# Kernel tuning notes

Hardware: AMD Instinct MI355X
Metric: run time of the kernel (lower is better)

The kernel has to match this reference:

```python
import jax, jax.numpy as jnp
import numpy as np

H, D = 4, 64          # num_heads, hidden_dim
NL, NP, B = 40000, 40000, 64
E_LL, E_LP, E_PL = 160000, 240000, 240000
NEG_SLOPE = 0.2


def _gat(x_src, x_dst, src, dst, Ws, Wd, al, ar, bias, n_dst):
    """DGL GATConv: fc -> edge score -> segment softmax over dst -> scatter-add."""
    fs = (x_src @ Ws).reshape(-1, H, D)            # [Ns,H,D]
    fd = (x_dst @ Wd).reshape(-1, H, D)            # [Nd,H,D]
    el = jnp.sum(fs * al, axis=-1)                 # [Ns,H]
    er = jnp.sum(fd * ar, axis=-1)                 # [Nd,H]
    e = jax.nn.leaky_relu(el[src] + er[dst], NEG_SLOPE)   # [E,H]
    m = jax.lax.stop_gradient(jax.ops.segment_max(e, dst, num_segments=n_dst))
    ex = jnp.exp(e - m[dst])
    s = jax.ops.segment_sum(ex, dst, num_segments=n_dst)
    a = ex / s[dst]                                # edge softmax over in-neighborhoods
    out = jax.ops.segment_sum(fs[src] * a[:, :, None], dst, num_segments=n_dst)
    return out + bias.reshape(1, H, D)


def _gmean(h, gid, nseg):
    s = jax.ops.segment_sum(h, gid, num_segments=nseg)
    c = jax.ops.segment_sum(jnp.ones((h.shape[0], 1), h.dtype), gid, num_segments=nseg)
    return s / jnp.maximum(c, 1.0)


_PARAM_SHAPES = [('W1_ll', (74, 256)), ('al1_ll', (H, D)), ('ar1_ll', (H, D)), ('b1_ll', (256,)),
                 ('W1_lps', (74, 256)), ('W1_lpd', (128, 256)), ('al1_lp', (H, D)), ('ar1_lp', (H, D)), ('b1_lp', (256,)),
                 ('W1_pls', (128, 256)), ('W1_pld', (74, 256)), ('al1_pl', (H, D)), ('ar1_pl', (H, D)), ('b1_pl', (256,)),
                 ('W2_ll', (256, 256)), ('al2_ll', (H, D)), ('ar2_ll', (H, D)), ('b2_ll', (256,)),
                 ('W2_lps', (256, 256)), ('W2_lpd', (256, 256)), ('al2_lp', (H, D)), ('ar2_lp', (H, D)), ('b2_lp', (256,)),
                 ('W2_pls', (256, 256)), ('W2_pld', (256, 256)), ('al2_pl', (H, D)), ('ar2_pl', (H, D)), ('b2_pl', (256,)),
                 ('W_mlp', (512, 256)), ('b_mlp', (256,))]


def setup_inputs() -> dict:
    key = jax.random.key(0)
    ks = iter(jax.random.split(key, 64))
    inp = {}
    inp['x_lig'] = jax.random.normal(next(ks), (NL, 74), jnp.float32)
    inp['x_pro'] = jax.random.normal(next(ks), (NP, 128), jnp.float32)
    for name, shape in _PARAM_SHAPES:
        inp[name] = jax.random.normal(next(ks), shape, jnp.float32) * 0.1
    inp['src_ll'] = jax.random.randint(next(ks), (E_LL,), 0, NL)
    inp['dst_ll'] = jax.random.randint(next(ks), (E_LL,), 0, NL)
    inp['src_lp'] = jax.random.randint(next(ks), (E_LP,), 0, NL)
    inp['dst_lp'] = jax.random.randint(next(ks), (E_LP,), 0, NP)
    inp['src_pl'] = jax.random.randint(next(ks), (E_PL,), 0, NP)
    inp['dst_pl'] = jax.random.randint(next(ks), (E_PL,), 0, NL)
    inp['gid_lig'] = jax.random.randint(next(ks), (NL,), 0, B)
    inp['gid_pro'] = jax.random.randint(next(ks), (NP,), 0, B)
    return inp


def reference(x_lig, x_pro, W1_ll, al1_ll, ar1_ll, b1_ll, W1_lps, W1_lpd, al1_lp, ar1_lp, b1_lp,
              W1_pls, W1_pld, al1_pl, ar1_pl, b1_pl, W2_ll, al2_ll, ar2_ll, b2_ll,
              W2_lps, W2_lpd, al2_lp, ar2_lp, b2_lp, W2_pls, W2_pld, al2_pl, ar2_pl, b2_pl,
              W_mlp, b_mlp, src_ll, dst_ll, src_lp, dst_lp, src_pl, dst_pl, gid_lig, gid_pro):
    # HeteroGraphConv layer 1 (aggregate='sum' over relations per dst ntype)
    h_l = (_gat(x_lig, x_lig, src_ll, dst_ll, W1_ll, W1_ll, al1_ll, ar1_ll, b1_ll, NL)
           + _gat(x_pro, x_lig, src_pl, dst_pl, W1_pls, W1_pld, al1_pl, ar1_pl, b1_pl, NL))
    h_p = _gat(x_lig, x_pro, src_lp, dst_lp, W1_lps, W1_lpd, al1_lp, ar1_lp, b1_lp, NP)
    h_l = jax.nn.relu(h_l.reshape(NL, H * D))
    h_p = jax.nn.relu(h_p.reshape(NP, H * D))
    # HeteroGraphConv layer 2
    h_l2 = (_gat(h_l, h_l, src_ll, dst_ll, W2_ll, W2_ll, al2_ll, ar2_ll, b2_ll, NL)
            + _gat(h_p, h_l, src_pl, dst_pl, W2_pls, W2_pld, al2_pl, ar2_pl, b2_pl, NL))
    h_p2 = _gat(h_l, h_p, src_lp, dst_lp, W2_lps, W2_lpd, al2_lp, ar2_lp, b2_lp, NP)
    h_l2 = jax.nn.relu(h_l2.reshape(NL, H * D))
    h_p2 = jax.nn.relu(h_p2.reshape(NP, H * D))
    # per-graph mean readout (dgl.mean_nodes) + concat + MLP (dropout=eval identity)
    g = jnp.concatenate([_gmean(h_l2, gid_lig, B), _gmean(h_p2, gid_pro, B)], axis=1)  # [B,512]
    return jax.nn.relu(g @ W_mlp + b_mlp)
```

## Files before the change

### kernel.cpp

```cpp
#include <hip/hip_runtime.h>
#include <hip/hip_bf16.h>

#define NLIG 40000
#define NPRO 40000
#define NGRAPH 64
#define ELL 160000
#define ELP 240000
#define EPL 240000

#define RD_STRIPES 256

typedef __hip_bfloat16 bf16;
typedef __attribute__((ext_vector_type(8))) short short8;
typedef __attribute__((ext_vector_type(4))) short short4v;
typedef __attribute__((ext_vector_type(4))) float f32x4;

__device__ __forceinline__ float bits2f(short s) {
  const unsigned u = ((unsigned)(unsigned short)s) << 16;
  return __uint_as_float(u);
}

__global__ __launch_bounds__(256) void convA_kernel(
    const float* __restrict__ A, bf16* __restrict__ hi, bf16* __restrict__ lo,
    int M, int K, int Kp) {
  const int row = blockIdx.x * 8 + (threadIdx.x >> 5);
  if (row >= M) return;
  const int Kp4 = Kp >> 2;
  short* hp = (short*)hi;
  short* lq = (short*)lo;
  for (int c4 = threadIdx.x & 31; c4 < Kp4; c4 += 32) {
    const int k = c4 << 2;
    float v[4];
#pragma unroll
    for (int j = 0; j < 4; ++j) {
      const int kk = k + j;
      v[j] = (kk < K) ? A[(size_t)row * K + kk] : 0.f;
    }
    short4v hv, lv;
#pragma unroll
    for (int j = 0; j < 4; ++j) {
      bf16 h = __float2bfloat16(v[j]);
      float r = v[j] - __bfloat162float(h);
      bf16 l = __float2bfloat16(r);
      hv[j] = *reinterpret_cast<short*>(&h);
      lv[j] = *reinterpret_cast<short*>(&l);
    }
    *reinterpret_cast<short4v*>(&hp[(size_t)row * Kp + k]) = hv;
    *reinterpret_cast<short4v*>(&lq[(size_t)row * Kp + k]) = lv;
  }
}

__global__ __launch_bounds__(256) void convBt_kernel(
    const float* __restrict__ B, bf16* __restrict__ thi, bf16* __restrict__ tlo,
    int K, int Kp) {
  const int tot = 256 * Kp;
  for (int i = blockIdx.x * 256 + threadIdx.x; i < tot; i += gridDim.x * 256) {
    const int n = i / Kp, k = i % Kp;
    float v = (k < K) ? B[(size_t)k * 256 + n] : 0.f;
    bf16 h = __float2bfloat16(v);
    float r = v - __bfloat162float(h);
    thi[i] = h;
    tlo[i] = __float2bfloat16(r);
  }
}

#define LP 40
__global__ __launch_bounds__(256) void mfma_gemm(
    const bf16* __restrict__ AhiP, const bf16* __restrict__ AloP,
    const bf16* __restrict__ BthiP, const bf16* __restrict__ BtloP,
    bf16* __restrict__ C, int M, int Kp,
    const float* __restrict__ al, float* __restrict__ el,
    const float* __restrict__ ar, float* __restrict__ er) {
  __shared__ short sA[2][128 * LP];
  __shared__ short sB[2][128 * LP];
  const short* Ahi = (const short*)AhiP;
  const short* Alo = (const short*)AloP;
  const short* Bthi = (const short*)BthiP;
  const short* Btlo = (const short*)BtloP;
  const int bid = blockIdx.x;
  const int rt = (bid >> 4) * 8 + (bid & 7);
  const int m0 = rt * 128;
  if (m0 >= M) return;
  const int n0 = ((bid >> 3) & 1) * 128;
  const int t = threadIdx.x;
  const int w = t >> 6, l = t & 63;
  const f32x4 zf = {0.f, 0.f, 0.f, 0.f};
  const short8 zs = {0, 0, 0, 0, 0, 0, 0, 0};
  f32x4 acc[2][8];
#pragma unroll
  for (int i = 0; i < 2; ++i)
#pragma unroll
    for (int j = 0; j < 8; ++j) acc[i][j] = zf;

  const int fr = l & 15, kg = l >> 4;

  for (int k0 = 0; k0 < Kp; k0 += 32) {
#pragma unroll
    for (int rep = 0; rep < 2; ++rep) {
      const int p = t + rep * 256;
      const int row = p >> 2, c = p & 3;
      const int gr = m0 + row;
      short8 vh = zs, vl = zs;
      if (gr < M) {
        const size_t g = (size_t)gr * Kp + k0 + c * 8;
        vh = *(const short8*)(Ahi + g);
        vl = *(const short8*)(Alo + g);
      }
      *(short8*)(&sA[0][row * LP + c * 8]) = vh;
      *(short8*)(&sA[1][row * LP + c * 8]) = vl;
    }
#pragma unroll
    for (int rep = 0; rep < 2; ++rep) {
      const int p = t + rep * 256;
      const int row = p >> 2, c = p & 3;
      const size_t g = (size_t)(n0 + row) * Kp + k0 + c * 8;
      *(short8*)(&sB[0][row * LP + c * 8]) = *(const short8*)(Bthi + g);
      *(short8*)(&sB[1][row * LP + c * 8]) = *(const short8*)(Btlo + g);
    }
    __syncthreads();
    short8 aF[2][2];
#pragma unroll
    for (int i = 0; i < 2; ++i) {
      const int r = (w * 32 + i * 16 + fr) * LP + kg * 8;
      aF[0][i] = *(const short8*)(&sA[0][r]);
      aF[1][i] = *(const short8*)(&sA[1][r]);
    }
#pragma unroll
    for (int j = 0; j < 8; ++j) {
      const int r = (j * 16 + fr) * LP + kg * 8;
      const short8 b0 = *(const short8*)(&sB[0][r]);
      const short8 b1 = *(const short8*)(&sB[1][r]);
#pragma unroll
      for (int i = 0; i < 2; ++i) {
        acc[i][j] = __builtin_amdgcn_mfma_f32_16x16x32_bf16(aF[0][i], b0, acc[i][j], 0, 0, 0);
        acc[i][j] = __builtin_amdgcn_mfma_f32_16x16x32_bf16(aF[0][i], b1, acc[i][j], 0, 0, 0);
        acc[i][j] = __builtin_amdgcn_mfma_f32_16x16x32_bf16(aF[1][i], b0, acc[i][j], 0, 0, 0);
      }
    }
    __syncthreads();
  }

#pragma unroll
  for (int i = 0; i < 2; ++i) {
    const int rbase = m0 + w * 32 + i * 16 + kg * 4;
#pragma unroll
    for (int j = 0; j < 8; ++j) {
      const int col = n0 + j * 16 + fr;
#pragma unroll
      for (int r = 0; r < 4; ++r) {
        const int row = rbase + r;
        if (row < M) C[(size_t)row * 256 + col] = __float2bfloat16(acc[i][j][r]);
      }
    }
  }

  if (el) {
    float alv[8], arv[8];
#pragma unroll
    for (int j = 0; j < 8; ++j) {
      alv[j] = al[n0 + j * 16 + fr];
      arv[j] = er ? ar[n0 + j * 16 + fr] : 0.f;
    }
    const int hb = n0 >> 6;
#pragma unroll
    for (int i = 0; i < 2; ++i) {
#pragma unroll
      for (int r = 0; r < 4; ++r) {
        float sl0 = 0.f, sl1 = 0.f, sr0 = 0.f, sr1 = 0.f;
#pragma unroll
        for (int j = 0; j < 4; ++j) {
          sl0 = fmaf(acc[i][j][r], alv[j], sl0);
          sr0 = fmaf(acc[i][j][r], arv[j], sr0);
          sl1 = fmaf(acc[i][j + 4][r], alv[j + 4], sl1);
          sr1 = fmaf(acc[i][j + 4][r], arv[j + 4], sr1);
        }
        sl0 += __shfl_xor(sl0, 1); sl0 += __shfl_xor(sl0, 2);
        sl0 += __shfl_xor(sl0, 4); sl0 += __shfl_xor(sl0, 8);
        sl1 += __shfl_xor(sl1, 1); sl1 += __shfl_xor(sl1, 2);
        sl1 += __shfl_xor(sl1, 4); sl1 += __shfl_xor(sl1, 8);
        sr0 += __shfl_xor(sr0, 1); sr0 += __shfl_xor(sr0, 2);
        sr0 += __shfl_xor(sr0, 4); sr0 += __shfl_xor(sr0, 8);
        sr1 += __shfl_xor(sr1, 1); sr1 += __shfl_xor(sr1, 2);
        sr1 += __shfl_xor(sr1, 4); sr1 += __shfl_xor(sr1, 8);
        const int row = m0 + w * 32 + i * 16 + kg * 4 + r;
        if (fr == 0 && row < M) {
          el[row * 4 + hb] = sl0;
          el[row * 4 + hb + 1] = sl1;
          if (er) {
            er[row * 4 + hb] = sr0;
            er[row * 4 + hb + 1] = sr1;
          }
        }
      }
    }
  }
}

__global__ void make_wr_kernel(const float* __restrict__ Wd,
                               const float* __restrict__ ar,
                               float* __restrict__ wr, int K) {
  const int t = blockIdx.x * blockDim.x + threadIdx.x;
  if (t < K * 4) {
    const int k = t >> 2, h = t & 3;
    float s = 0.f;
    for (int d = 0; d < 64; ++d)
      s = fmaf(Wd[(size_t)k * 256 + h * 64 + d], ar[h * 64 + d], s);
    wr[t] = s;
  }
}

__global__ __launch_bounds__(256) void er_gemv_kernel(
    const float* __restrict__ X, const float* __restrict__ wr,
    float* __restrict__ er, int n, int K) {
  __shared__ float swr[1024];
  const int t = threadIdx.x;
  for (int i = t; i < K * 4; i += blockDim.x) swr[i] = wr[i];
  __syncthreads();
  const int lane = t & 63;
  const int gw = (blockIdx.x * blockDim.x + t) >> 6;
  if (gw >= n) return;
  float a0 = 0.f, a1 = 0.f, a2 = 0.f, a3 = 0.f;
  for (int k = lane; k < K; k += 64) {
    const float x = X[(size_t)gw * K + k];
    a0 = fmaf(x, swr[k * 4 + 0], a0);
    a1 = fmaf(x, swr[k * 4 + 1], a1);
    a2 = fmaf(x, swr[k * 4 + 2], a2);
    a3 = fmaf(x, swr[k * 4 + 3], a3);
  }
#pragma unroll
  for (int o = 32; o; o >>= 1) {
    a0 += __shfl_xor(a0, o);
    a1 += __shfl_xor(a1, o);
    a2 += __shfl_xor(a2, o);
    a3 += __shfl_xor(a3, o);
  }
  if (lane == 0) {
    er[gw * 4 + 0] = a0; er[gw * 4 + 1] = a1;
    er[gw * 4 + 2] = a2; er[gw * 4 + 3] = a3;
  }
}

__global__ void count_kernel(const int* __restrict__ dst, int* __restrict__ cnt, int E) {
  for (int i = blockIdx.x * blockDim.x + threadIdx.x; i < E; i += gridDim.x * blockDim.x)
    atomicAdd(&cnt[dst[i]], 1);
}

__global__ __launch_bounds__(256) void scan_reduce_kernel(
    const int* __restrict__ data, int* __restrict__ bsum, int n) {
  const int base = blockIdx.x * 1024;
  int s = 0;
  for (int i = threadIdx.x; i < 1024; i += 256) {
    const int idx = base + i;
    s += (idx < n) ? data[idx] : 0;
  }
#pragma unroll
  for (int o = 32; o; o >>= 1) s += __shfl_xor(s, o);
  __shared__ int ws[4];
  if ((threadIdx.x & 63) == 0) ws[threadIdx.x >> 6] = s;
  __syncthreads();
  if (threadIdx.x == 0) bsum[blockIdx.x] = ws[0] + ws[1] + ws[2] + ws[3];
}

__global__ __launch_bounds__(1024) void scan_blocksums_kernel(
    int* __restrict__ bsum, int nb) {
  __shared__ int sm[1024];
  const int t = threadIdx.x;
  const int v = (t < nb) ? bsum[t] : 0;
  sm[t] = v;
  __syncthreads();
  for (int ofs = 1; ofs < 1024; ofs <<= 1) {
    const int tmp = (t >= ofs) ? sm[t - ofs] : 0;
    __syncthreads();
    sm[t] += tmp;
    __syncthreads();
  }
  if (t < nb) bsum[t] = sm[t] - v;
}

__global__ __launch_bounds__(1024) void scan_final_kernel(
    int* __restrict__ data, const int* __restrict__ bsum, int n) {
  __shared__ int sm[1024];
  const int t = threadIdx.x;
  const int i = blockIdx.x * 1024 + t;
  const int v = (i < n) ? data[i] : 0;
  sm[t] = v;
  __syncthreads();
  for (int ofs = 1; ofs < 1024; ofs <<= 1) {
    const int tmp = (t >= ofs) ? sm[t - ofs] : 0;
    __syncthreads();
    sm[t] += tmp;
    __syncthreads();
  }
  const int c = bsum[blockIdx.x];
  if (i < n) data[i] = c + sm[t] - v;
  if (i == n - 1) data[n] = c + sm[t];
}

__global__ void fill_kernel(const int* __restrict__ src, const int* __restrict__ dst,
                            const int* __restrict__ off, int* __restrict__ cursor,
                            int* __restrict__ csrsrc, int E) {
  for (int i = blockIdx.x * blockDim.x + threadIdx.x; i < E; i += gridDim.x * blockDim.x) {
    const int d = dst[i];
    const int p = atomicAdd(&cursor[d], 1);
    csrsrc[off[d] + p] = src[i];
  }
}

__device__ __forceinline__ float4 agg_walk(
    const short* __restrict__ Fp, const float* __restrict__ el, float ern,
    const int* __restrict__ csr, int s0, int s1, int myh, int lane) {
  float4 acc = {0.f, 0.f, 0.f, 0.f};
  float ssum = 0.f;
  for (int p = s0; p < s1; p += 8) {
    const int nb = s1 - p;
    int srcs[8];
#pragma unroll
    for (int b = 0; b < 8; ++b) {
      const int q = (b < nb) ? b : nb - 1;
      srcs[b] = csr[p + q];
    }
    float w8[8];
#pragma unroll
    for (int b = 0; b < 8; ++b) {
      float e = el[srcs[b] * 4 + myh] + ern;
      e = e > 0.f ? e : 0.2f * e;
      w8[b] = (b < nb) ? __expf(e) : 0.f;
    }
    short4v f8[8];
#pragma unroll
    for (int b = 0; b < 8; ++b)
      f8[b] = *reinterpret_cast<const short4v*>(&Fp[(size_t)srcs[b] * 256 + lane * 4]);
#pragma unroll
    for (int b = 0; b < 8; ++b) {
      ssum += w8[b];
      acc.x = fmaf(w8[b], bits2f(f8[b][0]), acc.x);
      acc.y = fmaf(w8[b], bits2f(f8[b][1]), acc.y);
      acc.z = fmaf(w8[b], bits2f(f8[b][2]), acc.z);
      acc.w = fmaf(w8[b], bits2f(f8[b][3]), acc.w);
    }
  }
  const float inv = ssum > 0.f ? 1.f / ssum : 0.f;
  float4 r = {acc.x * inv, acc.y * inv, acc.z * inv, acc.w * inv};
  return r;
}

__global__ __launch_bounds__(256) void gat_agg_fused(
    const bf16* __restrict__ F1, const float* __restrict__ el1,
    const float* __restrict__ er1, const int* __restrict__ off1,
    const int* __restrict__ csr1,
    const bf16* __restrict__ F2, const float* __restrict__ el2,
    const float* __restrict__ er2, const int* __restrict__ off2,
    const int* __restrict__ csr2,
    const float* __restrict__ bias1, const float* __restrict__ bias2,
    float* __restrict__ outF, bf16* __restrict__ outHi, bf16* __restrict__ outLo,
    const float* __restrict__ wr2, float* __restrict__ erOut,
    int n_dst) {
  const int lane = threadIdx.x & 63;
  const int myh = lane >> 4;
  const int gw = (blockIdx.x * blockDim.x + threadIdx.x) >> 6;
  if (gw >= n_dst) return;

  float4 res = agg_walk((const short*)F1, el1, er1[gw * 4 + myh],
                        csr1, off1[gw], off1[gw + 1], myh, lane);
  if (F2) {
    const float4 r2 = agg_walk((const short*)F2, el2, er2[gw * 4 + myh],
                               csr2, off2[gw], off2[gw + 1], myh, lane);
    res.x += r2.x; res.y += r2.y; res.z += r2.z; res.w += r2.w;
  }
  {
    float4 bb = *reinterpret_cast<const float4*>(&bias1[lane * 4]);
    if (bias2) {
      const float4 b2 = *reinterpret_cast<const float4*>(&bias2[lane * 4]);
      bb.x += b2.x; bb.y += b2.y; bb.z += b2.z; bb.w += b2.w;
    }
    res.x = fmaxf(res.x + bb.x, 0.f);
    res.y = fmaxf(res.y + bb.y, 0.f);
    res.z = fmaxf(res.z + bb.z, 0.f);
    res.w = fmaxf(res.w + bb.w, 0.f);
  }
  if (outF) {
    *reinterpret_cast<float4*>(&outF[(size_t)gw * 256 + lane * 4]) = res;
  } else {
    const float rv[4] = {res.x, res.y, res.z, res.w};
    short4v hv, lv;
#pragma unroll
    for (int j = 0; j < 4; ++j) {
      bf16 h = __float2bfloat16(rv[j]);
      float r = rv[j] - __bfloat162float(h);
      bf16 l = __float2bfloat16(r);
      hv[j] = *reinterpret_cast<const short*>(&h);
      lv[j] = *reinterpret_cast<const short*>(&l);
    }
    *reinterpret_cast<short4v*>(&((short*)outHi)[(size_t)gw * 256 + lane * 4]) = hv;
    *reinterpret_cast<short4v*>(&((short*)outLo)[(size_t)gw * 256 + lane * 4]) = lv;
  }
  if (erOut) {
    float4 wv0 = *reinterpret_cast<const float4*>(&wr2[(lane * 4 + 0) * 4]);
    float4 wv1 = *reinterpret_cast<const float4*>(&wr2[(lane * 4 + 1) * 4]);
    float4 wv2 = *reinterpret_cast<const float4*>(&wr2[(lane * 4 + 2) * 4]);
    float4 wv3 = *reinterpret_cast<const float4*>(&wr2[(lane * 4 + 3) * 4]);
    float e0 = res.x * wv0.x + res.y * wv1.x + res.z * wv2.x + res.w * wv3.x;
    float e1 = res.x * wv0.y + res.y * wv1.y + res.z * wv2.y + res.w * wv3.y;
    float e2 = res.x * wv0.z + res.y * wv1.z + res.z * wv2.z + res.w * wv3.z;
    float e3 = res.x * wv0.w + res.y * wv1.w + res.z * wv2.w + res.w * wv3.w;
#pragma unroll
    for (int o = 32; o; o >>= 1) {
      e0 += __shfl_xor(e0, o);
      e1 += __shfl_xor(e1, o);
      e2 += __shfl_xor(e2, o);
      e3 += __shfl_xor(e3, o);
    }
    if (lane == 0) {
      erOut[gw * 4 + 0] = e0; erOut[gw * 4 + 1] = e1;
      erOut[gw * 4 + 2] = e2; erOut[gw * 4 + 3] = e3;
    }
  }
}

__global__ __launch_bounds__(256) void graph_sum_v3(
    const float* __restrict__ h, const int* __restrict__ gid,
    float* __restrict__ pbuf, int n) {
  __shared__ float sm[NGRAPH * 256];
  const int t = threadIdx.x;
  for (int i = t; i < NGRAPH * 256; i += 256) sm[i] = 0.f;
  __syncthreads();
  const int chunk = (n + RD_STRIPES - 1) / RD_STRIPES;
  const int lo = blockIdx.x * chunk;
  const int hiN = min(n, lo + chunk);
#pragma unroll 8
  for (int node = lo; node < hiN; ++node) {
    const int g = gid[node];
    const float v = h[(size_t)node * 256 + t];
    sm[g * 256 + t] += v;
  }
  __syncthreads();
  float* dst = pbuf + (size_t)blockIdx.x * (NGRAPH * 256);
  for (int i = t; i < NGRAPH * 256; i += 256) dst[i] = sm[i];
}

__global__ __launch_bounds__(256) void graph_reduce_kernel(
    const float* __restrict__ pbuf, float* __restrict__ gsum, int colofs) {
  const int g = blockIdx.x, t = threadIdx.x;
  float acc = 0.f;
#pragma unroll 8
  for (int s = 0; s < RD_STRIPES; ++s)
    acc += pbuf[(size_t)s * (NGRAPH * 256) + g * 256 + t];
  gsum[(size_t)g * 512 + colofs + t] = acc;
}

__global__ __launch_bounds__(256) void graph_count_kernel(
    const int* __restrict__ gid, int* __restrict__ gcnt, int n, int cntofs) {
  __shared__ int c[NGRAPH];
  if (threadIdx.x < NGRAPH) c[threadIdx.x] = 0;
  __syncthreads();
  for (int i = blockIdx.x * blockDim.x + threadIdx.x; i < n; i += gridDim.x * blockDim.x)
    atomicAdd(&c[gid[i]], 1);
  __syncthreads();
  if (threadIdx.x < NGRAPH && c[threadIdx.x])
    atomicAdd(&gcnt[cntofs + threadIdx.x], c[threadIdx.x]);
}

__global__ __launch_bounds__(256) void mlp_kernel(
    const float* __restrict__ gsum, const int* __restrict__ gcnt,
    const float* __restrict__ Wm, const float* __restrict__ bm,
    float* __restrict__ out) {
  __shared__ float g[512];
  const int b = blockIdx.x, t = threadIdx.x;
  const float cl = fmaxf((float)gcnt[b], 1.f);
  const float cp = fmaxf((float)gcnt[64 + b], 1.f);
  for (int k = t; k < 512; k += 256)
    g[k] = gsum[(size_t)b * 512 + k] * (k < 256 ? 1.f / cl : 1.f / cp);
  __syncthreads();
  float acc = bm[t];
  for (int k = 0; k < 512; ++k) acc = fmaf(g[k], Wm[(size_t)k * 256 + t], acc);
  out[b * 256 + t] = fmaxf(acc, 0.f);
}

extern "C" void kernel_launch(void* const* d_in, const int* in_sizes, int n_in,
                              void* d_out, int out_size, void* d_ws, size_t ws_size,
                              hipStream_t stream) {
  const float* x_lig  = (const float*)d_in[0];
  const float* x_pro  = (const float*)d_in[1];
  const float* W1_ll  = (const float*)d_in[2];
  const float* al1_ll = (const float*)d_in[3];
  const float* ar1_ll = (const float*)d_in[4];
  const float* b1_ll  = (const float*)d_in[5];
  const float* W1_lps = (const float*)d_in[6];
  const float* W1_lpd = (const float*)d_in[7];
  const float* al1_lp = (const float*)d_in[8];
  const float* ar1_lp = (const float*)d_in[9];
  const float* b1_lp  = (const float*)d_in[10];
  const float* W1_pls = (const float*)d_in[11];
  const float* W1_pld = (const float*)d_in[12];
  const float* al1_pl = (const float*)d_in[13];
  const float* ar1_pl = (const float*)d_in[14];
  const float* b1_pl  = (const float*)d_in[15];
  const float* W2_ll  = (const float*)d_in[16];
  const float* al2_ll = (const float*)d_in[17];
  const float* ar2_ll = (const float*)d_in[18];
  const float* b2_ll  = (const float*)d_in[19];
  const float* W2_lps = (const float*)d_in[20];
  const float* W2_lpd = (const float*)d_in[21];
  const float* al2_lp = (const float*)d_in[22];
  const float* ar2_lp = (const float*)d_in[23];
  const float* b2_lp  = (const float*)d_in[24];
  const float* W2_pls = (const float*)d_in[25];
  const float* W2_pld = (const float*)d_in[26];
  const float* al2_pl = (const float*)d_in[27];
  const float* ar2_pl = (const float*)d_in[28];
  const float* b2_pl  = (const float*)d_in[29];
  const float* W_mlp  = (const float*)d_in[30];
  const float* b_mlp  = (const float*)d_in[31];
  const int* src_ll   = (const int*)d_in[32];
  const int* dst_ll   = (const int*)d_in[33];
  const int* src_lp   = (const int*)d_in[34];
  const int* dst_lp   = (const int*)d_in[35];
  const int* src_pl   = (const int*)d_in[36];
  const int* dst_pl   = (const int*)d_in[37];
  const int* gid_lig  = (const int*)d_in[38];
  const int* gid_pro  = (const int*)d_in[39];
  float* out = (float*)d_out;
  (void)in_sizes; (void)n_in; (void)out_size; (void)ws_size;

  size_t cur = 0;
  auto carve = [&](size_t bytes) -> char* {
    char* p = (char*)d_ws + cur;
    cur += (bytes + 511) & ~(size_t)511;
    return p;
  };
  const size_t NB   = (size_t)40000 * 256 * sizeof(float);
  const size_t NBH  = (size_t)40000 * 256 * sizeof(bf16);
  bf16* FbA   = (bf16*)carve(NBH);
  bf16* FbB   = (bf16*)carve(NBH);
  char* S1    = carve(NB);
  char* S2P   = carve(NB);
  float* hX   = (float*)carve(NB);
  float* elA  = (float*)carve((size_t)40000 * 4 * sizeof(float));
  float* erA  = (float*)carve((size_t)40000 * 4 * sizeof(float));
  float* elB  = (float*)carve((size_t)40000 * 4 * sizeof(float));
  float* erB  = (float*)carve((size_t)40000 * 4 * sizeof(float));
  float* erPL = (float*)carve((size_t)40000 * 4 * sizeof(float));
  float* erLP = (float*)carve((size_t)40000 * 4 * sizeof(float));
  float* wr1  = (float*)carve((size_t)256 * 4 * sizeof(float));
  float* wrA  = (float*)carve((size_t)256 * 4 * sizeof(float));
  float* wrB  = (float*)carve((size_t)256 * 4 * sizeof(float));
  bf16* Bthi  = (bf16*)carve((size_t)256 * 256 * sizeof(bf16));
  bf16* Btlo  = (bf16*)carve((size_t)256 * 256 * sizeof(bf16));
  float* gsum = (float*)carve((size_t)64 * 512 * sizeof(float));
  int* gcnt   = (int*)carve(128 * sizeof(int));
  int* bsum   = (int*)carve(1025 * sizeof(int));
  int* off_ll = (int*)carve((NLIG + 1) * sizeof(int));
  int* off_lp = (int*)carve((NPRO + 1) * sizeof(int));
  int* off_pl = (int*)carve((NLIG + 1) * sizeof(int));
  int* cursor = (int*)carve((NLIG + 1) * sizeof(int));
  int* csr_ll = (int*)carve((size_t)ELL * sizeof(int));
  int* csr_lp = (int*)carve((size_t)ELP * sizeof(int));
  int* csr_pl = (int*)carve((size_t)EPL * sizeof(int));

  bf16* XLhi = (bf16*)S1;
  bf16* XLlo = XLhi + (size_t)40000 * 96;
  bf16* XPhi = (bf16*)S2P;
  bf16* XPlo = XPhi + (size_t)40000 * 128;
  bf16* S1hi = (bf16*)S1;
  bf16* S1lo = S1hi + (size_t)40000 * 256;
  bf16* S2hi = (bf16*)S2P;
  bf16* S2lo = S2hi + (size_t)40000 * 256;
  float* P2  = (float*)S2P;
  float* pbuf = (float*)FbA;

  const int B256 = 256;
  auto thrGrid  = [](long long n) { return (int)((n + 255) / 256); };
  auto waveGrid = [](int n) { return (n + 3) / 4; };

  auto conv_a = [&](const float* A, bf16* hi, bf16* lo, int M, int K, int Kp) {
    convA_kernel<<<(M + 7) / 8, B256, 0, stream>>>(A, hi, lo, M, K, Kp);
  };
  auto run_mfma = [&](const bf16* ahi, const bf16* alo, const float* W, int K, int Kp,
                      bf16* C, int M, const float* alv, float* elp,
                      const float* arv, float* erp) {
    convBt_kernel<<<256, B256, 0, stream>>>(W, Bthi, Btlo, K, Kp);
    const int nrt = (M + 127) / 128;
    const int nb = ((nrt + 7) / 8) * 16;
    mfma_gemm<<<nb, B256, 0, stream>>>(ahi, alo, Bthi, Btlo, C, M, Kp, alv, elp, arv, erp);
  };
  auto run_scan = [&](int* data, int n) {
    const int nb = (n + 1023) / 1024;
    scan_reduce_kernel<<<nb, B256, 0, stream>>>(data, bsum, n);
    scan_blocksums_kernel<<<1, 1024, 0, stream>>>(bsum, nb);
    scan_final_kernel<<<nb, 1024, 0, stream>>>(data, bsum, n);
  };

  struct Rel { const int* src; const int* dst; int* off; int* csr; int E; int Nd; };
  Rel rels[3] = {
    {src_ll, dst_ll, off_ll, csr_ll, ELL, NLIG},
    {src_lp, dst_lp, off_lp, csr_lp, ELP, NPRO},
    {src_pl, dst_pl, off_pl, csr_pl, EPL, NLIG},
  };
  for (int r = 0; r < 3; ++r) {
    hipMemsetAsync(rels[r].off, 0, (rels[r].Nd + 1) * sizeof(int), stream);
    count_kernel<<<thrGrid(rels[r].E), B256, 0, stream>>>(rels[r].dst, rels[r].off, rels[r].E);
    run_scan(rels[r].off, rels[r].Nd);
    hipMemsetAsync(cursor, 0, (rels[r].Nd + 1) * sizeof(int), stream);
    fill_kernel<<<thrGrid(rels[r].E), B256, 0, stream>>>(
        rels[r].src, rels[r].dst, rels[r].off, cursor, rels[r].csr, rels[r].E);
  }

  conv_a(x_lig, XLhi, XLlo, NLIG, 74, 96);
  conv_a(x_pro, XPhi, XPlo, NPRO, 128, 128);
  run_mfma(XLhi, XLlo, W1_ll, 74, 96, FbA, NLIG, al1_ll, elA, ar1_ll, erA);
  run_mfma(XPhi, XPlo, W1_pls, 128, 128, FbB, NPRO, al1_pl, elB, nullptr, nullptr);
  make_wr_kernel<<<(74 * 4 + 255) / 256, B256, 0, stream>>>(W1_pld, ar1_pl, wr1, 74);
  er_gemv_kernel<<<waveGrid(NLIG), B256, 0, stream>>>(x_lig, wr1, erB, NLIG, 74);
  make_wr_kernel<<<(256 * 4 + 255) / 256, B256, 0, stream>>>(W2_pld, ar2_pl, wrA, 256);
  gat_agg_fused<<<waveGrid(NLIG), B256, 0, stream>>>(
      FbA, elA, erA, off_ll, csr_ll,
      FbB, elB, erB, off_pl, csr_pl,
      b1_ll, b1_pl, nullptr, S1hi, S1lo, wrA, erPL, NLIG);
  make_wr_kernel<<<(128 * 4 + 255) / 256, B256, 0, stream>>>(W1_lpd, ar1_lp, wr1, 128);
  er_gemv_kernel<<<waveGrid(NPRO), B256, 0, stream>>>(x_pro, wr1, erB, NPRO, 128);
  make_wr_kernel<<<(256 * 4 + 255) / 256, B256, 0, stream>>>(W2_lpd, ar2_lp, wrB, 256);
  conv_a(x_lig, XPhi, XPlo, NLIG, 74, 96);
  run_mfma(XPhi, XPlo, W1_lps, 74, 96, FbB, NLIG, al1_lp, elB, nullptr, nullptr);
  gat_agg_fused<<<waveGrid(NPRO), B256, 0, stream>>>(
      FbB, elB, erB, off_lp, csr_lp,
      nullptr, nullptr, nullptr, nullptr, nullptr,
      b1_lp, nullptr, nullptr, S2hi, S2lo, wrB, erLP, NPRO);

  run_mfma(S1hi, S1lo, W2_ll, 256, 256, FbA, NLIG, al2_ll, elA, ar2_ll, erA);
  run_mfma(S2hi, S2lo, W2_pls, 256, 256, FbB, NPRO, al2_pl, elB, nullptr, nullptr);
  gat_agg_fused<<<waveGrid(NLIG), B256, 0, stream>>>(
      FbA, elA, erA, off_ll, csr_ll,
      FbB, elB, erPL, off_pl, csr_pl,
      b2_ll, b2_pl, hX, nullptr, nullptr, nullptr, nullptr, NLIG);
  run_mfma(S1hi, S1lo, W2_lps, 256, 256, FbA, NLIG, al2_lp, elA, nullptr, nullptr);
  gat_agg_fused<<<waveGrid(NPRO), B256, 0, stream>>>(
      FbA, elA, erLP, off_lp, csr_lp,
      nullptr, nullptr, nullptr, nullptr, nullptr,
      b2_lp, nullptr, P2, nullptr, nullptr, nullptr, nullptr, NPRO);

  hipMemsetAsync(gcnt, 0, 128 * sizeof(int), stream);
  graph_sum_v3<<<RD_STRIPES, B256, 0, stream>>>(hX, gid_lig, pbuf, NLIG);
  graph_reduce_kernel<<<NGRAPH, B256, 0, stream>>>(pbuf, gsum, 0);
  graph_count_kernel<<<64, B256, 0, stream>>>(gid_lig, gcnt, NLIG, 0);
  graph_sum_v3<<<RD_STRIPES, B256, 0, stream>>>(P2, gid_pro, pbuf, NPRO);
  graph_reduce_kernel<<<NGRAPH, B256, 0, stream>>>(pbuf, gsum, 256);
  graph_count_kernel<<<64, B256, 0, stream>>>(gid_pro, gcnt, NPRO, 64);
  mlp_kernel<<<64, B256, 0, stream>>>(gsum, gcnt, W_mlp, b_mlp, out);
}
```

Before: 613.3 us.

## Merge same-input GEMMs into one wide launch and switch softmax to exp2

Both GEMMs that read ligand features (W_ll and W_lps, in each layer) now run as one 512-column MFMA launch writing to two output buffers. This removes a redundant convA pass, a separate GEMM launch and a second read of the A operand. The attention logits are pre-scaled by log2(e) in the GEMM epilogue and in make_wr, so the aggregation can use exp2f instead of __expf. The cost is an extra 20MB feature buffer plus a larger transposed weight buffer.

```diff
diff --git a/kernel.cpp b/kernel.cpp
--- a/kernel.cpp
+++ b/kernel.cpp
@@ -9,6 +9,7 @@
 #define EPL 240000
 
 #define RD_STRIPES 256
+#define LOG2E 1.44269504f
 
 typedef __hip_bfloat16 bf16;
 typedef __attribute__((ext_vector_type(8))) short short8;
@@ -68,9 +69,10 @@
 __global__ __launch_bounds__(256) void mfma_gemm(
     const bf16* __restrict__ AhiP, const bf16* __restrict__ AloP,
     const bf16* __restrict__ BthiP, const bf16* __restrict__ BtloP,
-    bf16* __restrict__ C, int M, int Kp,
-    const float* __restrict__ al, float* __restrict__ el,
-    const float* __restrict__ ar, float* __restrict__ er) {
+    bf16* __restrict__ C0, bf16* __restrict__ C1, int M, int Kp, int log2ncb,
+    const float* __restrict__ al0, float* __restrict__ el0,
+    const float* __restrict__ ar0, float* __restrict__ er0,
+    const float* __restrict__ al1, float* __restrict__ el1) {
   __shared__ short sA[2][128 * LP];
   __shared__ short sB[2][128 * LP];
   const short* Ahi = (const short*)AhiP;
@@ -78,10 +80,11 @@
   const short* Bthi = (const short*)BthiP;
   const short* Btlo = (const short*)BtloP;
   const int bid = blockIdx.x;
-  const int rt = (bid >> 4) * 8 + (bid & 7);
+  const int ncb = 1 << log2ncb;
+  const int rt = (bid >> (3 + log2ncb)) * 8 + (bid & 7);
   const int m0 = rt * 128;
   if (m0 >= M) return;
-  const int n0 = ((bid >> 3) & 1) * 128;
+  const int n0 = ((bid >> 3) & (ncb - 1)) * 128;
   const int t = threadIdx.x;
   const int w = t >> 6, l = t & 63;
   const f32x4 zf = {0.f, 0.f, 0.f, 0.f};
@@ -140,12 +143,19 @@
     __syncthreads();
   }
 
+  bf16* C = (n0 < 256) ? C0 : C1;
+  const int nloc = n0 & 255;
+  const float* alp = (n0 < 256) ? al0 : al1;
+  const float* arp = (n0 < 256) ? ar0 : nullptr;
+  float* elp = (n0 < 256) ? el0 : el1;
+  float* erp = (n0 < 256) ? er0 : nullptr;
+
 #pragma unroll
   for (int i = 0; i < 2; ++i) {
     const int rbase = m0 + w * 32 + i * 16 + kg * 4;
 #pragma unroll
     for (int j = 0; j < 8; ++j) {
-      const int col = n0 + j * 16 + fr;
+      const int col = nloc + j * 16 + fr;
 #pragma unroll
       for (int r = 0; r < 4; ++r) {
         const int row = rbase + r;
@@ -154,14 +164,14 @@
     }
   }
 
-  if (el) {
+  if (elp) {
     float alv[8], arv[8];
 #pragma unroll
     for (int j = 0; j < 8; ++j) {
-      alv[j] = al[n0 + j * 16 + fr];
-      arv[j] = er ? ar[n0 + j * 16 + fr] : 0.f;
-    }
-    const int hb = n0 >> 6;
+      alv[j] = alp[nloc + j * 16 + fr] * LOG2E;
+      arv[j] = (arp && erp) ? arp[nloc + j * 16 + fr] * LOG2E : 0.f;
+    }
+    const int hb = nloc >> 6;
 #pragma unroll
     for (int i = 0; i < 2; ++i) {
 #pragma unroll
@@ -184,11 +194,11 @@
         sr1 += __shfl_xor(sr1, 4); sr1 += __shfl_xor(sr1, 8);
         const int row = m0 + w * 32 + i * 16 + kg * 4 + r;
         if (fr == 0 && row < M) {
-          el[row * 4 + hb] = sl0;
-          el[row * 4 + hb + 1] = sl1;
-          if (er) {
-            er[row * 4 + hb] = sr0;
-            er[row * 4 + hb + 1] = sr1;
+          elp[row * 4 + hb] = sl0;
+          elp[row * 4 + hb + 1] = sl1;
+          if (erp) {
+            erp[row * 4 + hb] = sr0;
+            erp[row * 4 + hb + 1] = sr1;
           }
         }
       }
@@ -205,7 +215,7 @@
     float s = 0.f;
     for (int d = 0; d < 64; ++d)
       s = fmaf(Wd[(size_t)k * 256 + h * 64 + d], ar[h * 64 + d], s);
-    wr[t] = s;
+    wr[t] = s * LOG2E;
   }
 }
 
@@ -324,7 +334,7 @@
     for (int b = 0; b < 8; ++b) {
       float e = el[srcs[b] * 4 + myh] + ern;
       e = e > 0.f ? e : 0.2f * e;
-      w8[b] = (b < nb) ? __expf(e) : 0.f;
+      w8[b] = (b < nb) ? exp2f(e) : 0.f;
     }
     short4v f8[8];
 #pragma unroll
@@ -532,6 +542,7 @@
   const size_t NBH  = (size_t)40000 * 256 * sizeof(bf16);
   bf16* FbA   = (bf16*)carve(NBH);
   bf16* FbB   = (bf16*)carve(NBH);
+  bf16* FbC   = (bf16*)carve(NBH);
   char* S1    = carve(NB);
   char* S2P   = carve(NB);
   float* hX   = (float*)carve(NB);
@@ -539,13 +550,14 @@
   float* erA  = (float*)carve((size_t)40000 * 4 * sizeof(float));
   float* elB  = (float*)carve((size_t)40000 * 4 * sizeof(float));
   float* erB  = (float*)carve((size_t)40000 * 4 * sizeof(float));
+  float* elC  = (float*)carve((size_t)40000 * 4 * sizeof(float));
   float* erPL = (float*)carve((size_t)40000 * 4 * sizeof(float));
   float* erLP = (float*)carve((size_t)40000 * 4 * sizeof(float));
   float* wr1  = (float*)carve((size_t)256 * 4 * sizeof(float));
   float* wrA  = (float*)carve((size_t)256 * 4 * sizeof(float));
   float* wrB  = (float*)carve((size_t)256 * 4 * sizeof(float));
-  bf16* Bthi  = (bf16*)carve((size_t)256 * 256 * sizeof(bf16));
-  bf16* Btlo  = (bf16*)carve((size_t)256 * 256 * sizeof(bf16));
+  bf16* Bthi  = (bf16*)carve((size_t)512 * 256 * sizeof(bf16));
+  bf16* Btlo  = (bf16*)carve((size_t)512 * 256 * sizeof(bf16));
   float* gsum = (float*)carve((size_t)64 * 512 * sizeof(float));
   int* gcnt   = (int*)carve(128 * sizeof(int));
   int* bsum   = (int*)carve(1025 * sizeof(int));
@@ -575,13 +587,20 @@
   auto conv_a = [&](const float* A, bf16* hi, bf16* lo, int M, int K, int Kp) {
     convA_kernel<<<(M + 7) / 8, B256, 0, stream>>>(A, hi, lo, M, K, Kp);
   };
-  auto run_mfma = [&](const bf16* ahi, const bf16* alo, const float* W, int K, int Kp,
-                      bf16* C, int M, const float* alv, float* elp,
-                      const float* arv, float* erp) {
-    convBt_kernel<<<256, B256, 0, stream>>>(W, Bthi, Btlo, K, Kp);
+  auto run_mfma = [&](const bf16* ahi, const bf16* alo,
+                      const float* Wa, const float* Wb, int K, int Kp, int M,
+                      bf16* C0, bf16* C1,
+                      const float* al0, float* el0, const float* ar0, float* er0,
+                      const float* al1, float* el1) {
+    convBt_kernel<<<256, B256, 0, stream>>>(Wa, Bthi, Btlo, K, Kp);
+    if (Wb)
+      convBt_kernel<<<256, B256, 0, stream>>>(Wb, Bthi + (size_t)256 * Kp,
+                                              Btlo + (size_t)256 * Kp, K, Kp);
+    const int log2ncb = Wb ? 2 : 1;
     const int nrt = (M + 127) / 128;
-    const int nb = ((nrt + 7) / 8) * 16;
-    mfma_gemm<<<nb, B256, 0, stream>>>(ahi, alo, Bthi, Btlo, C, M, Kp, alv, elp, arv, erp);
+    const int nb = ((nrt + 7) / 8) * 8 * (1 << log2ncb);
+    mfma_gemm<<<nb, B256, 0, stream>>>(ahi, alo, Bthi, Btlo, C0, C1, M, Kp, log2ncb,
+                                       al0, el0, ar0, er0, al1, el1);
   };
   auto run_scan = [&](int* data, int n) {
     const int nb = (n + 1023) / 1024;
@@ -607,34 +626,35 @@
 
   conv_a(x_lig, XLhi, XLlo, NLIG, 74, 96);
   conv_a(x_pro, XPhi, XPlo, NPRO, 128, 128);
-  run_mfma(XLhi, XLlo, W1_ll, 74, 96, FbA, NLIG, al1_ll, elA, ar1_ll, erA);
-  run_mfma(XPhi, XPlo, W1_pls, 128, 128, FbB, NPRO, al1_pl, elB, nullptr, nullptr);
+  run_mfma(XLhi, XLlo, W1_ll, W1_lps, 74, 96, NLIG,
+           FbA, FbC, al1_ll, elA, ar1_ll, erA, al1_lp, elC);
+  run_mfma(XPhi, XPlo, W1_pls, nullptr, 128, 128, NPRO,
+           FbB, nullptr, al1_pl, elB, nullptr, nullptr, nullptr, nullptr);
   make_wr_kernel<<<(74 * 4 + 255) / 256, B256, 0, stream>>>(W1_pld, ar1_pl, wr1, 74);
   er_gemv_kernel<<<waveGrid(NLIG), B256, 0, stream>>>(x_lig, wr1, erB, NLIG, 74);
   make_wr_kernel<<<(256 * 4 + 255) / 256, B256, 0, stream>>>(W2_pld, ar2_pl, wrA, 256);
+  make_wr_kernel<<<(256 * 4 + 255) / 256, B256, 0, stream>>>(W2_lpd, ar2_lp, wrB, 256);
   gat_agg_fused<<<waveGrid(NLIG), B256, 0, stream>>>(
       FbA, elA, erA, off_ll, csr_ll,
       FbB, elB, erB, off_pl, csr_pl,
       b1_ll, b1_pl, nullptr, S1hi, S1lo, wrA, erPL, NLIG);
   make_wr_kernel<<<(128 * 4 + 255) / 256, B256, 0, stream>>>(W1_lpd, ar1_lp, wr1, 128);
   er_gemv_kernel<<<waveGrid(NPRO), B256, 0, stream>>>(x_pro, wr1, erB, NPRO, 128);
-  make_wr_kernel<<<(256 * 4 + 255) / 256, B256, 0, stream>>>(W2_lpd, ar2_lp, wrB, 256);
-  conv_a(x_lig, XPhi, XPlo, NLIG, 74, 96);
-  run_mfma(XPhi, XPlo, W1_lps, 74, 96, FbB, NLIG, al1_lp, elB, nullptr, nullptr);
   gat_agg_fused<<<waveGrid(NPRO), B256, 0, stream>>>(
-      FbB, elB, erB, off_lp, csr_lp,
+      FbC, elC, erB, off_lp, csr_lp,
       nullptr, nullptr, nullptr, nullptr, nullptr,
       b1_lp, nullptr, nullptr, S2hi, S2lo, wrB, erLP, NPRO);
 
-  run_mfma(S1hi, S1lo, W2_ll, 256, 256, FbA, NLIG, al2_ll, elA, ar2_ll, erA);
-  run_mfma(S2hi, S2lo, W2_pls, 256, 256, FbB, NPRO, al2_pl, elB, nullptr, nullptr);
+  run_mfma(S1hi, S1lo, W2_ll, W2_lps, 256, 256, NLIG,
+           FbA, FbC, al2_ll, elA, ar2_ll, erA, al2_lp, elC);
+  run_mfma(S2hi, S2lo, W2_pls, nullptr, 256, 256, NPRO,
+           FbB, nullptr, al2_pl, elB, nullptr, nullptr, nullptr, nullptr);
   gat_agg_fused<<<waveGrid(NLIG), B256, 0, stream>>>(
       FbA, elA, erA, off_ll, csr_ll,
       FbB, elB, erPL, off_pl, csr_pl,
       b2_ll, b2_pl, hX, nullptr, nullptr, nullptr, nullptr, NLIG);
-  run_mfma(S1hi, S1lo, W2_lps, 256, 256, FbA, NLIG, al2_lp, elA, nullptr, nullptr);
   gat_agg_fused<<<waveGrid(NPRO), B256, 0, stream>>>(
-      FbA, elA, erLP, off_lp, csr_lp,
+      FbC, elC, erLP, off_lp, csr_lp,
       nullptr, nullptr, nullptr, nullptr, nullptr,
       b2_lp, nullptr, P2, nullptr, nullptr, nullptr, nullptr, NPRO);
 
```

Measured after the change: 594.3 us, median of 2. 3.1% less time.
